# Kernel tuning notes

Measured on AMD Instinct MI355X. Metric: run time of the kernel, lower is better.

Reference implementation:

```python
import jax, jax.numpy as jnp
import numpy as np

SR = 16000
N_FFT = 1024
HOP = 160
N_MELS = 160
F_MIN = 50.0
F_MAX = 4000.0
SEG = 32000
N_FREQS = N_FFT // 2 + 1  # 513


def _hz_to_mel(f):
    return 2595.0 * np.log10(1.0 + f / 700.0)


def _mel_to_hz(m):
    return 700.0 * (10.0 ** (m / 2595.0) - 1.0)


def _mel_filterbank():
    # replicates torchaudio melscale_fbanks (htk, norm=None); returns (n_mels, n_freqs)
    all_freqs = np.linspace(0.0, SR / 2.0, N_FREQS)
    m_pts = np.linspace(_hz_to_mel(F_MIN), _hz_to_mel(F_MAX), N_MELS + 2)
    f_pts = _mel_to_hz(m_pts)
    slopes = f_pts[None, :] - all_freqs[:, None]          # (n_freqs, n_mels+2)
    down = -slopes[:, :-2] / (f_pts[1:-1] - f_pts[:-2])
    up = slopes[:, 2:] / (f_pts[2:] - f_pts[1:-1])
    fb = np.maximum(0.0, np.minimum(down, up))            # (n_freqs, n_mels)
    return fb.T.astype(np.float32)


def _dft_matrices():
    k = np.arange(N_FREQS).reshape(-1, 1)
    n = np.arange(N_FFT).reshape(1, -1)
    angle = 2.0 * np.pi * k * n / N_FFT
    return np.cos(angle).astype(np.float32), (-np.sin(angle)).astype(np.float32)


def setup_inputs() -> dict:
    key = jax.random.key(0)
    waveform = jax.random.normal(key, (256, SEG), dtype=jnp.float32)
    # periodic hann window (torch.hann_window default)
    n = np.arange(N_FFT)
    window = (0.5 * (1.0 - np.cos(2.0 * np.pi * n / N_FFT))).astype(np.float32)
    dft_real, dft_imag = _dft_matrices()
    return {
        "waveform": waveform,
        "window": jnp.asarray(window),
        "dft_real": jnp.asarray(dft_real),   # (513, 1024)
        "dft_imag": jnp.asarray(dft_imag),   # (513, 1024)
        "mel_fb": jnp.asarray(_mel_filterbank()),  # (160, 513)
    }


def reference(waveform, window, dft_real, dft_imag, mel_fb):
    pad = N_FFT // 2
    x = jnp.pad(waveform, ((0, 0), (pad, pad)), mode="reflect")  # (B, 33024)
    num_frames = (x.shape[1] - N_FFT) // HOP + 1                  # 201
    idx = np.arange(num_frames)[:, None] * HOP + np.arange(N_FFT)[None, :]
    frames = x[:, idx]                                            # (B, T, n_fft)
    fw = frames * window[None, None, :]
    real = jnp.einsum('btn,fn->btf', fw, dft_real)                # (B, T, 513)
    imag = jnp.einsum('btn,fn->btf', fw, dft_imag)
    power = real * real + imag * imag
    mel = jnp.einsum('btf,mf->btm', power, mel_fb)                # (B, T, n_mels)
    return jnp.transpose(mel, (0, 2, 1))                          # (B, n_mels, T)
```

## Files before the change

kernel.cpp:

```cpp
#include <hip/hip_runtime.h>
#include <stdint.h>

#define NFFT    1024
#define HOP     160
#define NMELS   160
#define SEG     32000
#define PADW    512
#define NFRAMES 201
#define NBATCH  256
#define FBW     12
#define NSTEP   32
#define ROWB    336
#define NROWS   230
#define WPCH    (NROWS * 21)
#define WPB2    (WPCH * 8)
#define FILLCH  2496

using bf16x8 = __attribute__((ext_vector_type(8))) __bf16;
using f32x4  = __attribute__((ext_vector_type(4))) float;

static __device__ __forceinline__ uint16_t f2bf(float f) {
    union { float f; uint32_t u; } v; v.f = f;
    return (uint16_t)((v.u + 0x7FFFu + ((v.u >> 16) & 1u)) >> 16);
}
static __device__ __forceinline__ void gload16(const void* g, void* l) {
    __builtin_amdgcn_global_load_lds(
        (const __attribute__((address_space(1))) uint32_t*)(uintptr_t)g,
        (__attribute__((address_space(3))) uint32_t*)(uintptr_t)l,
        16, 0, 0);
}

#define PAD_BLKS  (NBATCH * 19)
#define BTF_BLKS  256
#define FBT_BLKS  20
#define PREP_GRID (PAD_BLKS + BTF_BLKS + FBT_BLKS)

__global__ void k_prep(const float* __restrict__ wav, const float* __restrict__ win,
                       const float* __restrict__ dre, const float* __restrict__ dimg,
                       const float* __restrict__ mfb,
                       uint16_t* __restrict__ wp2, uint16_t* __restrict__ BTf,
                       uint16_t* __restrict__ fbT) {
    int bid = blockIdx.x, tid = threadIdx.x;
    if (bid < PAD_BLKS) {
        int b = bid / 19, ib = bid - b * 19;
        int chunk = ib * 256 + tid;
        if (chunk >= WPCH) return;
        int row = chunk / 21, cc = chunk - row * 21;
        uint16_t r[8] = {0,0,0,0,0,0,0,0};
        if (cc < 20) {
            int s0 = row * 160 + cc * 8;
            if (s0 >= PADW && s0 + 8 <= PADW + SEG) {
                const float* s = wav + (size_t)b * SEG + (s0 - PADW);
                float4 v0 = *(const float4*)s;
                float4 v1 = *(const float4*)(s + 4);
                r[0]=f2bf(v0.x); r[1]=f2bf(v0.y); r[2]=f2bf(v0.z); r[3]=f2bf(v0.w);
                r[4]=f2bf(v1.x); r[5]=f2bf(v1.y); r[6]=f2bf(v1.z); r[7]=f2bf(v1.w);
            } else {
                #pragma unroll
                for (int e = 0; e < 8; ++e) {
                    int i = s0 + e - PADW;
                    int j = (i < 0) ? -i : ((i >= SEG) ? (2 * SEG - 2 - i) : i);
                    r[e] = f2bf(wav[(size_t)b * SEG + j]);
                }
            }
        }
        *(uint4*)(wp2 + (size_t)b * WPB2 + (size_t)chunk * 8) = *(const uint4*)r;
    } else if (bid < PAD_BLKS + BTF_BLKS) {
        int idx8 = (bid - PAD_BLKS) * 256 + tid;
        int lane  = idx8 & 63;
        int kstep = (idx8 >> 6) & 31;
        int ntile = (idx8 >> 11) & 15;
        int mat   = idx8 >> 15;
        int bin = ntile * 16 + (lane & 15);
        int k0  = kstep * 32 + (lane >> 4) * 8;
        const float* src = (mat ? dimg : dre) + (size_t)bin * 1024 + k0;
        const float* w   = win + k0;
        uint16_t r[8];
        #pragma unroll
        for (int j = 0; j < 8; ++j) r[j] = f2bf(src[j] * w[j]);
        *(uint4*)(BTf + (size_t)idx8 * 8) = *(const uint4*)r;
    } else {
        int idx = (bid - PAD_BLKS - BTF_BLKS) * 256 + tid;
        if (idx >= 5120) return;
        int lane = idx & 63;
        int fI = idx >> 6;
        int kf = fI & 7, mt = fI >> 3;
        int mel = mt * 16 + (lane & 15);
        int b0  = kf * 32 + (lane >> 4) * 8;
        const float* s = mfb + (size_t)mel * 513 + b0;
        uint16_t r[8];
        #pragma unroll
        for (int j = 0; j < 8; ++j) r[j] = f2bf(s[j]);
        *(uint4*)(fbT + (size_t)idx * 8) = *(const uint4*)r;
    }
}

__global__ __launch_bounds__(512, 1) void k_main(
    const uint16_t* __restrict__ wp2, const uint16_t* __restrict__ BTf,
    const uint16_t* __restrict__ fbT, float* __restrict__ out)
{
    __shared__ uint4 smem4[57344 / 16];
    char* smem = (char*)smem4;

    const int tid  = threadIdx.x;
    const int lane = tid & 63;
    const int wn   = tid >> 6;
    const int l15 = lane & 15, lg = lane >> 4;
    const int b    = blockIdx.x;
    const int h    = blockIdx.y;
    const int r0   = h ? 96 : 0;

    const uint16_t* wsrc = wp2 + (size_t)b * WPB2 + (size_t)r0 * 168;
    #pragma unroll
    for (int i = 0; i < 4; ++i)
        gload16(wsrc + (size_t)(tid + i * 512) * 8, smem + (size_t)(tid + i * 512) * 16);
    if (tid < FILLCH - 2048)
        gload16(wsrc + (size_t)(tid + 2048) * 8, smem + (size_t)(tid + 2048) * 16);
    asm volatile("s_waitcnt vmcnt(0)" ::: "memory");
    __syncthreads();

    const uint32_t alane = (uint32_t)(l15 * ROWB + lg * 16);
    const uint16_t* bp = BTf + (size_t)(wn * 2) * 16384 + lane * 8;

    f32x4 acc[7][4];
    #pragma unroll
    for (int fi = 0; fi < 7; ++fi)
        #pragma unroll
        for (int nf = 0; nf < 4; ++nf)
            acc[fi][nf] = f32x4{0.f, 0.f, 0.f, 0.f};

    bf16x8 bvA[4], bvB[4], bvC[4], av[7];

    #define LOADB(dst, t) { \
        dst[0] = *(const bf16x8*)(bp + (size_t)(t) * 512); \
        dst[1] = *(const bf16x8*)(bp + 16384 + (size_t)(t) * 512); \
        dst[2] = *(const bf16x8*)(bp + 262144 + (size_t)(t) * 512); \
        dst[3] = *(const bf16x8*)(bp + 278528 + (size_t)(t) * 512); }
    #define LOADA(t) { \
        const uint32_t aoff_ = (uint32_t)(((t) / 5) * ROWB + ((32 * (t)) % 160) * 2); \
        _Pragma("unroll") \
        for (int fi = 0; fi < 7; ++fi) \
            av[fi] = *(const bf16x8*)(smem + alane + aoff_ + (uint32_t)(fi * 16 * ROWB)); }
    #define MFMA28(bv) { \
        _Pragma("unroll") \
        for (int fi = 0; fi < 7; ++fi) \
            _Pragma("unroll") \
            for (int nf = 0; nf < 4; ++nf) \
                acc[fi][nf] = __builtin_amdgcn_mfma_f32_16x16x32_bf16( \
                    av[fi], bv[nf], acc[fi][nf], 0, 0, 0); }

    LOADB(bvA, 0);
    LOADB(bvB, 1);
    #pragma unroll
    for (int t = 0; t < NSTEP; ++t) {
        LOADA(t);
        if (t + 2 < NSTEP) {
            const int n2 = (t + 2) % 3;
            if      (n2 == 0) { LOADB(bvA, t + 2); }
            else if (n2 == 1) { LOADB(bvB, t + 2); }
            else              { LOADB(bvC, t + 2); }
        }
        const int c = t % 3;
        if      (c == 0) { MFMA28(bvA); }
        else if (c == 1) { MFMA28(bvB); }
        else             { MFMA28(bvC); }
    }
    __syncthreads();

    uint16_t* pw16 = (uint16_t*)smem;
    #pragma unroll
    for (int fi = 0; fi < 7; ++fi)
        #pragma unroll
        for (int nt = 0; nt < 2; ++nt)
            #pragma unroll
            for (int e = 0; e < 4; ++e) {
                const int frow = fi * 16 + lg * 4 + e;
                const int bin  = (wn * 2 + nt) * 16 + l15;
                float r = acc[fi][nt][e], im = acc[fi][nt + 2][e];
                const int slot = ((bin >> 3) + frow) & 31;
                *(uint16_t*)(smem + frow * 512 + slot * 16 + (bin & 7) * 2)
                    = f2bf(r * r + im * im);
            }
    __syncthreads();

    float* obase = out + (size_t)b * (NMELS * NFRAMES);
    for (int task = wn; task < 70; task += 8) {
        const int mt = task / 7, ft = task - mt * 7;
        f32x4 d = f32x4{0.f, 0.f, 0.f, 0.f};
        const int frame = ft * 16 + l15;
        #pragma unroll
        for (int kf = 0; kf < 8; ++kf) {
            bf16x8 a = *(const bf16x8*)(fbT + (size_t)((mt * 8 + kf) * 64 + lane) * 8);
            const int slot = (kf * 4 + lg + frame) & 31;
            bf16x8 bb = *(const bf16x8*)(smem + frame * 512 + slot * 16);
            d = __builtin_amdgcn_mfma_f32_16x16x32_bf16(a, bb, d, 0, 0, 0);
        }
        const int fg = r0 + frame;
        const bool own = h ? (fg >= 104 && fg <= 200) : (fg <= 103);
        if (own) {
            #pragma unroll
            for (int e = 0; e < 4; ++e)
                obase[(mt * 16 + lg * 4 + e) * NFRAMES + fg] = d[e];
        }
    }
}

extern "C" void kernel_launch(void* const* d_in, const int* in_sizes, int n_in,
                              void* d_out, int out_size, void* d_ws, size_t ws_size,
                              hipStream_t stream) {
    const float* wav  = (const float*)d_in[0];
    const float* win  = (const float*)d_in[1];
    const float* dre  = (const float*)d_in[2];
    const float* dimg = (const float*)d_in[3];
    const float* mfb  = (const float*)d_in[4];
    float* out = (float*)d_out;

    uint8_t* ws = (uint8_t*)d_ws;
    uint16_t* BTf = (uint16_t*)ws;
    uint16_t* wp2 = (uint16_t*)(ws + (1u << 20));
    size_t off = (1u << 20) + (size_t)NBATCH * WPB2 * 2;
    uint16_t* fbT = (uint16_t*)(ws + off);

    hipLaunchKernelGGL(k_prep, dim3(PREP_GRID), dim3(256), 0, stream,
                       wav, win, dre, dimg, mfb, wp2, BTf, fbT);
    hipLaunchKernelGGL(k_main, dim3(NBATCH, 2), dim3(512), 0, stream,
                       wp2, BTf, fbT, out);
}
```

Before: 80.06 us.

## Exploit DFT even/odd symmetry to halve the STFT GEMM reduction depth

Uses the cos/sin symmetry around the frame midpoint: each frame is folded into sum and difference halves (x[n]±x[N-n]), and the real and imaginary parts are computed with only 512 reduction taps instead of 1024. This halves the MFMA work and the DFT-basis loads. A reversed copy of the waveform rows is built in LDS, and the n=512 term is added back separately with an alternating sign. The cost is more LDS use (about 97KB), extra VALU conversions before every MFMA, and a reversal pass before the main loop.

Measured after the change: 92.51 us. 1.16x slower.

```diff
diff --git a/kernel.cpp b/kernel.cpp
--- a/kernel.cpp
+++ b/kernel.cpp
@@ -8,20 +8,27 @@
 #define PADW    512
 #define NFRAMES 201
 #define NBATCH  256
-#define FBW     12
-#define NSTEP   32
+#define NSTEP   16
 #define ROWB    336
 #define NROWS   230
 #define WPCH    (NROWS * 21)
 #define WPB2    (WPCH * 8)
 #define FILLCH  2496
+#define YOFF    39648
+#define PW_OFF  39648
+#define LDS_TOTAL 96992
 
 using bf16x8 = __attribute__((ext_vector_type(8))) __bf16;
 using f32x4  = __attribute__((ext_vector_type(4))) float;
+using u32x4v = __attribute__((ext_vector_type(4))) unsigned int;
 
 static __device__ __forceinline__ uint16_t f2bf(float f) {
     union { float f; uint32_t u; } v; v.f = f;
     return (uint16_t)((v.u + 0x7FFFu + ((v.u >> 16) & 1u)) >> 16);
+}
+static __device__ __forceinline__ float bf2f(uint16_t h) {
+    union { uint32_t u; float f; } v; v.u = (uint32_t)h << 16;
+    return v.f;
 }
 static __device__ __forceinline__ void gload16(const void* g, void* l) {
     __builtin_amdgcn_global_load_lds(
@@ -31,14 +38,14 @@
 }
 
 #define PAD_BLKS  (NBATCH * 19)
-#define BTF_BLKS  256
+#define BTFS_BLKS 128
 #define FBT_BLKS  20
-#define PREP_GRID (PAD_BLKS + BTF_BLKS + FBT_BLKS)
+#define PREP_GRID (PAD_BLKS + BTFS_BLKS + FBT_BLKS)
 
 __global__ void k_prep(const float* __restrict__ wav, const float* __restrict__ win,
                        const float* __restrict__ dre, const float* __restrict__ dimg,
                        const float* __restrict__ mfb,
-                       uint16_t* __restrict__ wp2, uint16_t* __restrict__ BTf,
+                       uint16_t* __restrict__ wp2, uint16_t* __restrict__ BTfs,
                        uint16_t* __restrict__ fbT) {
     int bid = blockIdx.x, tid = threadIdx.x;
     if (bid < PAD_BLKS) {
@@ -65,12 +72,12 @@
             }
         }
         *(uint4*)(wp2 + (size_t)b * WPB2 + (size_t)chunk * 8) = *(const uint4*)r;
-    } else if (bid < PAD_BLKS + BTF_BLKS) {
+    } else if (bid < PAD_BLKS + BTFS_BLKS) {
         int idx8 = (bid - PAD_BLKS) * 256 + tid;
         int lane  = idx8 & 63;
-        int kstep = (idx8 >> 6) & 31;
-        int ntile = (idx8 >> 11) & 15;
-        int mat   = idx8 >> 15;
+        int kstep = (idx8 >> 6) & 15;
+        int ntile = (idx8 >> 10) & 15;
+        int mat   = idx8 >> 14;
         int bin = ntile * 16 + (lane & 15);
         int k0  = kstep * 32 + (lane >> 4) * 8;
         const float* src = (mat ? dimg : dre) + (size_t)bin * 1024 + k0;
@@ -78,9 +85,9 @@
         uint16_t r[8];
         #pragma unroll
         for (int j = 0; j < 8; ++j) r[j] = f2bf(src[j] * w[j]);
-        *(uint4*)(BTf + (size_t)idx8 * 8) = *(const uint4*)r;
+        *(uint4*)(BTfs + (size_t)idx8 * 8) = *(const uint4*)r;
     } else {
-        int idx = (bid - PAD_BLKS - BTF_BLKS) * 256 + tid;
+        int idx = (bid - PAD_BLKS - BTFS_BLKS) * 256 + tid;
         if (idx >= 5120) return;
         int lane = idx & 63;
         int fI = idx >> 6;
@@ -96,10 +103,10 @@
 }
 
 __global__ __launch_bounds__(512, 1) void k_main(
-    const uint16_t* __restrict__ wp2, const uint16_t* __restrict__ BTf,
+    const uint16_t* __restrict__ wp2, const uint16_t* __restrict__ BTfs,
     const uint16_t* __restrict__ fbT, float* __restrict__ out)
 {
-    __shared__ uint4 smem4[57344 / 16];
+    __shared__ uint4 smem4[LDS_TOTAL / 16];
     char* smem = (char*)smem4;
 
     const int tid  = threadIdx.x;
@@ -119,8 +126,22 @@
     asm volatile("s_waitcnt vmcnt(0)" ::: "memory");
     __syncthreads();
 
+    for (int ch = tid; ch < 115 * 20; ch += 512) {
+        int q = ch / 20, c = ch - q * 20;
+        int s0 = 160 * q + 544 - 8 * c;
+        int sA = s0 - 8;
+        uint4 A = *(const uint4*)(smem + (sA / 160) * ROWB + (sA % 160) * 2);
+        uint4 B = *(const uint4*)(smem + (s0 / 160) * ROWB + (s0 % 160) * 2);
+        uint32_t d0 = (B.x & 0xffffu) | (A.w & 0xffff0000u);
+        uint32_t d1 = (A.w & 0xffffu) | (A.z & 0xffff0000u);
+        uint32_t d2 = (A.z & 0xffffu) | (A.y & 0xffff0000u);
+        uint32_t d3 = (A.y & 0xffffu) | (A.x & 0xffff0000u);
+        *(uint4*)(smem + YOFF + q * ROWB + c * 16) = uint4{d0, d1, d2, d3};
+    }
+    __syncthreads();
+
     const uint32_t alane = (uint32_t)(l15 * ROWB + lg * 16);
-    const uint16_t* bp = BTf + (size_t)(wn * 2) * 16384 + lane * 8;
+    const uint16_t* bp = BTfs + (size_t)(wn * 2) * 8192 + lane * 8;
 
     f32x4 acc[7][4];
     #pragma unroll
@@ -129,31 +150,42 @@
         for (int nf = 0; nf < 4; ++nf)
             acc[fi][nf] = f32x4{0.f, 0.f, 0.f, 0.f};
 
-    bf16x8 bvA[4], bvB[4], bvC[4], av[7];
+    bf16x8 bvA[4], bvB[4], bvC[4];
 
     #define LOADB(dst, t) { \
         dst[0] = *(const bf16x8*)(bp + (size_t)(t) * 512); \
-        dst[1] = *(const bf16x8*)(bp + 16384 + (size_t)(t) * 512); \
-        dst[2] = *(const bf16x8*)(bp + 262144 + (size_t)(t) * 512); \
-        dst[3] = *(const bf16x8*)(bp + 278528 + (size_t)(t) * 512); }
-    #define LOADA(t) { \
-        const uint32_t aoff_ = (uint32_t)(((t) / 5) * ROWB + ((32 * (t)) % 160) * 2); \
+        dst[1] = *(const bf16x8*)(bp + 8192 + (size_t)(t) * 512); \
+        dst[2] = *(const bf16x8*)(bp + 131072 + (size_t)(t) * 512); \
+        dst[3] = *(const bf16x8*)(bp + 131072 + 8192 + (size_t)(t) * 512); }
+
+    #define FORM_MFMA(fi, t, bv) { \
+        u32x4v xf = *(const u32x4v*)(smem + alane + \
+            (uint32_t)((fi) * 16 * ROWB + ((t) / 5) * ROWB + ((32 * (t)) % 160) * 2)); \
+        u32x4v xr = *(const u32x4v*)(smem + alane + \
+            (uint32_t)(YOFF + ((fi) * 16 + 3 - (t) / 5) * ROWB + ((32 * (t)) % 160) * 2)); \
+        bf16x8 uu, vv; \
         _Pragma("unroll") \
-        for (int fi = 0; fi < 7; ++fi) \
-            av[fi] = *(const bf16x8*)(smem + alane + aoff_ + (uint32_t)(fi * 16 * ROWB)); }
-    #define MFMA28(bv) { \
-        _Pragma("unroll") \
-        for (int fi = 0; fi < 7; ++fi) \
-            _Pragma("unroll") \
-            for (int nf = 0; nf < 4; ++nf) \
-                acc[fi][nf] = __builtin_amdgcn_mfma_f32_16x16x32_bf16( \
-                    av[fi], bv[nf], acc[fi][nf], 0, 0, 0); }
+        for (int d = 0; d < 4; ++d) { \
+            float alo = __uint_as_float(xf[d] << 16); \
+            float ahi = __uint_as_float(xf[d] & 0xffff0000u); \
+            float blo = __uint_as_float(xr[d] << 16); \
+            float bhi = __uint_as_float(xr[d] & 0xffff0000u); \
+            float ulo = alo + blo, uhi = ahi + bhi; \
+            float vlo = alo - blo, vhi = ahi - bhi; \
+            uint32_t ud, vd; \
+            asm("v_cvt_pk_bf16_f32 %0, %1, %2" : "=v"(ud) : "v"(ulo), "v"(uhi)); \
+            asm("v_cvt_pk_bf16_f32 %0, %1, %2" : "=v"(vd) : "v"(vlo), "v"(vhi)); \
+            ((u32x4v*)&uu)[0][d] = ud; ((u32x4v*)&vv)[0][d] = vd; \
+        } \
+        acc[fi][0] = __builtin_amdgcn_mfma_f32_16x16x32_bf16(uu, bv[0], acc[fi][0], 0, 0, 0); \
+        acc[fi][1] = __builtin_amdgcn_mfma_f32_16x16x32_bf16(uu, bv[1], acc[fi][1], 0, 0, 0); \
+        acc[fi][2] = __builtin_amdgcn_mfma_f32_16x16x32_bf16(vv, bv[2], acc[fi][2], 0, 0, 0); \
+        acc[fi][3] = __builtin_amdgcn_mfma_f32_16x16x32_bf16(vv, bv[3], acc[fi][3], 0, 0, 0); }
 
     LOADB(bvA, 0);
     LOADB(bvB, 1);
     #pragma unroll
     for (int t = 0; t < NSTEP; ++t) {
-        LOADA(t);
         if (t + 2 < NSTEP) {
             const int n2 = (t + 2) % 3;
             if      (n2 == 0) { LOADB(bvA, t + 2); }
@@ -161,26 +193,32 @@
             else              { LOADB(bvC, t + 2); }
         }
         const int c = t % 3;
-        if      (c == 0) { MFMA28(bvA); }
-        else if (c == 1) { MFMA28(bvB); }
-        else             { MFMA28(bvC); }
-    }
-    __syncthreads();
-
-    uint16_t* pw16 = (uint16_t*)smem;
+        #pragma unroll
+        for (int fi = 0; fi < 7; ++fi) {
+            if      (c == 0) { FORM_MFMA(fi, t, bvA); }
+            else if (c == 1) { FORM_MFMA(fi, t, bvB); }
+            else             { FORM_MFMA(fi, t, bvC); }
+        }
+    }
+    __syncthreads();
+
+    const float sgn = (l15 & 1) ? -1.f : 1.f;
     #pragma unroll
     for (int fi = 0; fi < 7; ++fi)
         #pragma unroll
-        for (int nt = 0; nt < 2; ++nt)
+        for (int e = 0; e < 4; ++e) {
+            const int frow = fi * 16 + lg * 4 + e;
+            const float c512 = bf2f(*(const uint16_t*)(smem + (frow + 3) * ROWB + 64));
             #pragma unroll
-            for (int e = 0; e < 4; ++e) {
-                const int frow = fi * 16 + lg * 4 + e;
-                const int bin  = (wn * 2 + nt) * 16 + l15;
-                float r = acc[fi][nt][e], im = acc[fi][nt + 2][e];
+            for (int nt = 0; nt < 2; ++nt) {
+                const int bin = (wn * 2 + nt) * 16 + l15;
+                float r  = acc[fi][nt][e] + sgn * c512;
+                float im = acc[fi][nt + 2][e];
                 const int slot = ((bin >> 3) + frow) & 31;
-                *(uint16_t*)(smem + frow * 512 + slot * 16 + (bin & 7) * 2)
+                *(uint16_t*)(smem + PW_OFF + frow * 512 + slot * 16 + (bin & 7) * 2)
                     = f2bf(r * r + im * im);
             }
+        }
     __syncthreads();
 
     float* obase = out + (size_t)b * (NMELS * NFRAMES);
@@ -192,7 +230,7 @@
         for (int kf = 0; kf < 8; ++kf) {
             bf16x8 a = *(const bf16x8*)(fbT + (size_t)((mt * 8 + kf) * 64 + lane) * 8);
             const int slot = (kf * 4 + lg + frame) & 31;
-            bf16x8 bb = *(const bf16x8*)(smem + frame * 512 + slot * 16);
+            bf16x8 bb = *(const bf16x8*)(smem + PW_OFF + frame * 512 + slot * 16);
             d = __builtin_amdgcn_mfma_f32_16x16x32_bf16(a, bb, d, 0, 0, 0);
         }
         const int fg = r0 + frame;
@@ -216,13 +254,13 @@
     float* out = (float*)d_out;
 
     uint8_t* ws = (uint8_t*)d_ws;
-    uint16_t* BTf = (uint16_t*)ws;
-    uint16_t* wp2 = (uint16_t*)(ws + (1u << 20));
+    uint16_t* BTfs = (uint16_t*)ws;
+    uint16_t* wp2  = (uint16_t*)(ws + (1u << 20));
     size_t off = (1u << 20) + (size_t)NBATCH * WPB2 * 2;
     uint16_t* fbT = (uint16_t*)(ws + off);
 
     hipLaunchKernelGGL(k_prep, dim3(PREP_GRID), dim3(256), 0, stream,
-                       wav, win, dre, dimg, mfb, wp2, BTf, fbT);
+                       wav, win, dre, dimg, mfb, wp2, BTfs, fbT);
     hipLaunchKernelGGL(k_main, dim3(NBATCH, 2), dim3(512), 0, stream,
-                       wp2, BTf, fbT, out);
-}
+                       wp2, BTfs, fbT, out);
+}
```

## Double workgroup to 16 waves, each computing one frequency tile

Applied to the files above, without the earlier changes.

Launches the main kernel with 1024 threads instead of 512, so each of 16 waves owns one 16-bin frequency tile (real and imaginary) instead of two. Per-wave accumulators and B-operand registers shrink, and the explicit triple-buffered B prefetch is dropped in favour of direct loads each step. The aim is more waves per CU to hide global-load latency. The cost is that each A fragment read from LDS is reused over fewer MFMAs, doubling LDS A traffic, and there is no explicit software pipelining of the B loads.

Result: no change. 80.87 us (+1.0%).

```diff
diff --git a/kernel.cpp b/kernel.cpp
--- a/kernel.cpp
+++ b/kernel.cpp
@@ -8,7 +8,6 @@
 #define PADW    512
 #define NFRAMES 201
 #define NBATCH  256
-#define FBW     12
 #define NSTEP   32
 #define ROWB    336
 #define NROWS   230
@@ -95,7 +94,7 @@
     }
 }
 
-__global__ __launch_bounds__(512, 1) void k_main(
+__global__ __launch_bounds__(1024, 1) void k_main(
     const uint16_t* __restrict__ wp2, const uint16_t* __restrict__ BTf,
     const uint16_t* __restrict__ fbT, float* __restrict__ out)
 {
@@ -111,80 +110,55 @@
     const int r0   = h ? 96 : 0;
 
     const uint16_t* wsrc = wp2 + (size_t)b * WPB2 + (size_t)r0 * 168;
-    #pragma unroll
-    for (int i = 0; i < 4; ++i)
-        gload16(wsrc + (size_t)(tid + i * 512) * 8, smem + (size_t)(tid + i * 512) * 16);
+    gload16(wsrc + (size_t)tid * 8,          smem + (size_t)tid * 16);
+    gload16(wsrc + (size_t)(tid + 1024) * 8, smem + (size_t)(tid + 1024) * 16);
     if (tid < FILLCH - 2048)
         gload16(wsrc + (size_t)(tid + 2048) * 8, smem + (size_t)(tid + 2048) * 16);
     asm volatile("s_waitcnt vmcnt(0)" ::: "memory");
     __syncthreads();
 
     const uint32_t alane = (uint32_t)(l15 * ROWB + lg * 16);
-    const uint16_t* bp = BTf + (size_t)(wn * 2) * 16384 + lane * 8;
-
-    f32x4 acc[7][4];
+    const uint16_t* bp = BTf + (size_t)wn * 16384 + lane * 8;
+
+    f32x4 acc[7][2];
+    #pragma unroll
+    for (int fi = 0; fi < 7; ++fi) {
+        acc[fi][0] = f32x4{0.f, 0.f, 0.f, 0.f};
+        acc[fi][1] = f32x4{0.f, 0.f, 0.f, 0.f};
+    }
+
+    #pragma unroll
+    for (int t = 0; t < NSTEP; ++t) {
+        bf16x8 bvR = *(const bf16x8*)(bp + (size_t)t * 512);
+        bf16x8 bvI = *(const bf16x8*)(bp + 262144 + (size_t)t * 512);
+        const uint32_t aoff = (uint32_t)((t / 5) * ROWB + ((32 * t) % 160) * 2);
+        bf16x8 av[7];
+        #pragma unroll
+        for (int fi = 0; fi < 7; ++fi)
+            av[fi] = *(const bf16x8*)(smem + alane + aoff + (uint32_t)(fi * 16 * ROWB));
+        #pragma unroll
+        for (int fi = 0; fi < 7; ++fi) {
+            acc[fi][0] = __builtin_amdgcn_mfma_f32_16x16x32_bf16(av[fi], bvR, acc[fi][0], 0, 0, 0);
+            acc[fi][1] = __builtin_amdgcn_mfma_f32_16x16x32_bf16(av[fi], bvI, acc[fi][1], 0, 0, 0);
+        }
+    }
+    __syncthreads();
+
     #pragma unroll
     for (int fi = 0; fi < 7; ++fi)
         #pragma unroll
-        for (int nf = 0; nf < 4; ++nf)
-            acc[fi][nf] = f32x4{0.f, 0.f, 0.f, 0.f};
-
-    bf16x8 bvA[4], bvB[4], bvC[4], av[7];
-
-    #define LOADB(dst, t) { \
-        dst[0] = *(const bf16x8*)(bp + (size_t)(t) * 512); \
-        dst[1] = *(const bf16x8*)(bp + 16384 + (size_t)(t) * 512); \
-        dst[2] = *(const bf16x8*)(bp + 262144 + (size_t)(t) * 512); \
-        dst[3] = *(const bf16x8*)(bp + 278528 + (size_t)(t) * 512); }
-    #define LOADA(t) { \
-        const uint32_t aoff_ = (uint32_t)(((t) / 5) * ROWB + ((32 * (t)) % 160) * 2); \
-        _Pragma("unroll") \
-        for (int fi = 0; fi < 7; ++fi) \
-            av[fi] = *(const bf16x8*)(smem + alane + aoff_ + (uint32_t)(fi * 16 * ROWB)); }
-    #define MFMA28(bv) { \
-        _Pragma("unroll") \
-        for (int fi = 0; fi < 7; ++fi) \
-            _Pragma("unroll") \
-            for (int nf = 0; nf < 4; ++nf) \
-                acc[fi][nf] = __builtin_amdgcn_mfma_f32_16x16x32_bf16( \
-                    av[fi], bv[nf], acc[fi][nf], 0, 0, 0); }
-
-    LOADB(bvA, 0);
-    LOADB(bvB, 1);
-    #pragma unroll
-    for (int t = 0; t < NSTEP; ++t) {
-        LOADA(t);
-        if (t + 2 < NSTEP) {
-            const int n2 = (t + 2) % 3;
-            if      (n2 == 0) { LOADB(bvA, t + 2); }
-            else if (n2 == 1) { LOADB(bvB, t + 2); }
-            else              { LOADB(bvC, t + 2); }
-        }
-        const int c = t % 3;
-        if      (c == 0) { MFMA28(bvA); }
-        else if (c == 1) { MFMA28(bvB); }
-        else             { MFMA28(bvC); }
-    }
+        for (int e = 0; e < 4; ++e) {
+            const int frow = fi * 16 + lg * 4 + e;
+            const int bin  = wn * 16 + l15;
+            float r = acc[fi][0][e], im = acc[fi][1][e];
+            const int slot = ((bin >> 3) + frow) & 31;
+            *(uint16_t*)(smem + frow * 512 + slot * 16 + (bin & 7) * 2)
+                = f2bf(r * r + im * im);
+        }
     __syncthreads();
 
-    uint16_t* pw16 = (uint16_t*)smem;
-    #pragma unroll
-    for (int fi = 0; fi < 7; ++fi)
-        #pragma unroll
-        for (int nt = 0; nt < 2; ++nt)
-            #pragma unroll
-            for (int e = 0; e < 4; ++e) {
-                const int frow = fi * 16 + lg * 4 + e;
-                const int bin  = (wn * 2 + nt) * 16 + l15;
-                float r = acc[fi][nt][e], im = acc[fi][nt + 2][e];
-                const int slot = ((bin >> 3) + frow) & 31;
-                *(uint16_t*)(smem + frow * 512 + slot * 16 + (bin & 7) * 2)
-                    = f2bf(r * r + im * im);
-            }
-    __syncthreads();
-
     float* obase = out + (size_t)b * (NMELS * NFRAMES);
-    for (int task = wn; task < 70; task += 8) {
+    for (int task = wn; task < 70; task += 16) {
         const int mt = task / 7, ft = task - mt * 7;
         f32x4 d = f32x4{0.f, 0.f, 0.f, 0.f};
         const int frame = ft * 16 + l15;
@@ -223,6 +197,6 @@
 
     hipLaunchKernelGGL(k_prep, dim3(PREP_GRID), dim3(256), 0, stream,
                        wav, win, dre, dimg, mfb, wp2, BTf, fbT);
-    hipLaunchKernelGGL(k_main, dim3(NBATCH, 2), dim3(512), 0, stream,
+    hipLaunchKernelGGL(k_main, dim3(NBATCH, 2), dim3(1024), 0, stream,
                        wp2, BTf, fbT, out);
 }
```
